# Optimization experiments

Measured on AMD Instinct MI355X. Metric: run time of the kernel, lower is better.

Reference implementation:

```python
import jax, jax.numpy as jnp
import numpy as np

N_USER = 150000
N_RECIPE = 150000
H = 64        # hidden_channels
UF = 58       # user_feat_dim
RF = 128      # recipe_feat_dim
E = 2000000   # rating edges
EL = 500000   # supervision edges


def _lin(k, fan_out, fan_in):
    s = 1.0 / np.sqrt(fan_in)
    kw, kb = jax.random.split(k)
    w = jax.random.uniform(kw, (fan_out, fan_in), jnp.float32, -s, s)
    b = jax.random.uniform(kb, (fan_out,), jnp.float32, -s, s)
    return w, b


def setup_inputs() -> dict:
    key = jax.random.key(0)
    ks = jax.random.split(key, 16)
    inp = {
        'x_user': jax.random.normal(ks[0], (N_USER, UF), jnp.float32),
        'x_recipe': jax.random.normal(ks[1], (N_RECIPE, RF), jnp.float32),
        'user_node_id': jnp.arange(N_USER, dtype=jnp.int64 if jax.config.jax_enable_x64 else jnp.int32),
        'recipe_node_id': jnp.arange(N_RECIPE, dtype=jnp.int64 if jax.config.jax_enable_x64 else jnp.int32),
        'edge_index': jax.random.randint(ks[2], (2, E), 0, N_USER),
        'edge_label_index': jax.random.randint(ks[3], (2, EL), 0, N_USER),
    }
    inp['user_lin_w'], inp['user_lin_b'] = _lin(ks[4], H, UF)
    inp['recipe_lin_w'], inp['recipe_lin_b'] = _lin(ks[5], H, RF)
    inp['user_emb'] = jax.random.normal(ks[6], (N_USER, H), jnp.float32)
    inp['recipe_emb'] = jax.random.normal(ks[7], (N_RECIPE, H), jnp.float32)
    # SAGEConv per layer (1,2) per relation (rates: user->recipe, rev: recipe->user)
    i = 8
    for layer in (1, 2):
        for rel in ('rates', 'rev'):
            wl, bl = _lin(ks[i], H, H)
            wr, _ = _lin(ks[i + 1], H, H)  # lin_r has no bias in PyG SAGEConv
            inp[f'c{layer}_{rel}_wl'] = wl
            inp[f'c{layer}_{rel}_bl'] = bl
            inp[f'c{layer}_{rel}_wr'] = wr
            i += 2
    return inp


def sage_conv(x_src, x_dst, src, dst, wl, bl, wr, n_dst):
    # PyG SAGEConv: lin_l(mean of neighbor messages) + lin_r(self)
    msg = x_src[src]                                              # [E, H] gather
    summed = jax.ops.segment_sum(msg, dst, num_segments=n_dst)    # [n_dst, H]
    cnt = jax.ops.segment_sum(jnp.ones((src.shape[0],), x_src.dtype), dst,
                              num_segments=n_dst)
    mean = summed / jnp.maximum(cnt, 1.0)[:, None]
    return mean @ wl.T + bl + x_dst @ wr.T


def reference(x_user, x_recipe, user_node_id, recipe_node_id, edge_index,
              edge_label_index, user_lin_w, user_lin_b, recipe_lin_w,
              recipe_lin_b, user_emb, recipe_emb,
              c1_rates_wl, c1_rates_bl, c1_rates_wr,
              c1_rev_wl, c1_rev_bl, c1_rev_wr,
              c2_rates_wl, c2_rates_bl, c2_rates_wr,
              c2_rev_wl, c2_rev_bl, c2_rev_wr):
    # Input encoders: linear + embedding lookup
    xu = x_user @ user_lin_w.T + user_lin_b + user_emb[user_node_id]
    xr = x_recipe @ recipe_lin_w.T + recipe_lin_b + recipe_emb[recipe_node_id]

    u_src, r_dst = edge_index[0], edge_index[1]

    # Layer 1 (hetero: each node type receives from exactly one relation)
    hr = sage_conv(xu, xr, u_src, r_dst, c1_rates_wl, c1_rates_bl, c1_rates_wr, N_RECIPE)
    hu = sage_conv(xr, xu, r_dst, u_src, c1_rev_wl, c1_rev_bl, c1_rev_wr, N_USER)
    hu, hr = jax.nn.relu(hu), jax.nn.relu(hr)

    # Layer 2
    hr2 = sage_conv(hu, hr, u_src, r_dst, c2_rates_wl, c2_rates_bl, c2_rates_wr, N_RECIPE)
    hu2 = sage_conv(hr, hu, r_dst, u_src, c2_rev_wl, c2_rev_bl, c2_rev_wr, N_USER)

    # Dot-product edge classifier
    return (hu2[edge_label_index[0]] * hr2[edge_label_index[1]]).sum(axis=-1)
```

## Files before the change

kernel.cpp:

```cpp
#include <hip/hip_runtime.h>
#include <hip/hip_fp16.h>

constexpr int NU = 150000;
constexpr int NR = 150000;
constexpr int Hc = 64;
constexpr int UF = 58;
constexpr int RF = 128;
constexpr long EE = 2000000;
constexpr long ELc = 500000;
constexpr int NTOT = NU + NR;
constexpr int BKT = 256;
constexpr int NB_R = (NR + BKT - 1) / BKT;
constexpr int NB_U = (NU + BKT - 1) / BKT;
constexpr int NBKT = NB_R + NB_U;
constexpr int CHUNK = 4096;
constexpr int NCHUNK = (int)((EE + CHUNK - 1) / CHUNK);
constexpr int NTILE = NU / 16;
constexpr int GB8 = (NU / 8 + 3) / 4;

typedef _Float16 f16;
typedef f16 f16x8 __attribute__((ext_vector_type(8)));
typedef float f32x4 __attribute__((ext_vector_type(4)));

__global__ void bucket_count_kernel(const int* __restrict__ ei, int* __restrict__ bcnt) {
    __shared__ int lc[NBKT];
    for (int i = threadIdx.x; i < NBKT; i += 256) lc[i] = 0;
    __syncthreads();
    long e0 = (long)blockIdx.x * CHUNK;
    for (int k = threadIdx.x; k < CHUNK; k += 256) {
        long e = e0 + k;
        if (e < EE) {
            int u = ei[e], r = ei[EE + e];
            atomicAdd(&lc[r >> 8], 1);
            atomicAdd(&lc[NB_R + (u >> 8)], 1);
        }
    }
    __syncthreads();
    for (int i = threadIdx.x; i < NBKT; i += 256)
        if (lc[i]) atomicAdd(&bcnt[i], lc[i]);
}

__global__ void bucket_scan_kernel(const int* __restrict__ bcnt, int* __restrict__ bbase,
                                   int* __restrict__ bcur) {
    __shared__ int part[256];
    constexpr int PER = (NBKT + 255) / 256;
    int t = threadIdx.x;
    int loc[PER];
    int sum = 0;
    for (int j = 0; j < PER; ++j) {
        int i = t * PER + j;
        int v = (i < NBKT) ? bcnt[i] : 0;
        loc[j] = sum;
        sum += v;
    }
    part[t] = sum;
    __syncthreads();
    for (int off = 1; off < 256; off <<= 1) {
        int v = (t >= off) ? part[t - off] : 0;
        __syncthreads();
        part[t] += v;
        __syncthreads();
    }
    int pre = (t == 0) ? 0 : part[t - 1];
    for (int j = 0; j < PER; ++j) {
        int i = t * PER + j;
        if (i < NBKT) {
            int b = pre + loc[j];
            bbase[i] = b;
            bcur[i] = b;
        }
    }
    if (t == 255) bbase[NBKT] = part[255];
}

__global__ void scatter_records_kernel(const int* __restrict__ ei, int* __restrict__ bcur,
                                       int* __restrict__ rec) {
    __shared__ int lc[NBKT];
    for (int i = threadIdx.x; i < NBKT; i += 256) lc[i] = 0;
    __syncthreads();
    long e0 = (long)blockIdx.x * CHUNK;
    for (int k = threadIdx.x; k < CHUNK; k += 256) {
        long e = e0 + k;
        if (e < EE) {
            int u = ei[e], r = ei[EE + e];
            atomicAdd(&lc[r >> 8], 1);
            atomicAdd(&lc[NB_R + (u >> 8)], 1);
        }
    }
    __syncthreads();
    for (int i = threadIdx.x; i < NBKT; i += 256) {
        int c = lc[i];
        lc[i] = c ? atomicAdd(&bcur[i], c) : 0;
    }
    __syncthreads();
    for (int k = threadIdx.x; k < CHUNK; k += 256) {
        long e = e0 + k;
        if (e < EE) {
            int u = ei[e], r = ei[EE + e];
            int p1 = atomicAdd(&lc[r >> 8], 1);
            rec[p1] = ((r & 255) << 18) | u;
            int p2 = atomicAdd(&lc[NB_R + (u >> 8)], 1);
            rec[p2] = ((u & 255) << 18) | r;
        }
    }
}

__global__ void build_adj_kernel(const int* __restrict__ rec, const int* __restrict__ bbase,
                                 int* __restrict__ adj, int* __restrict__ base,
                                 int* __restrict__ cnt) {
    __shared__ int c256[BKT];
    __shared__ int off256[BKT];
    int b = blockIdx.x;
    int s = bbase[b], e = bbase[b + 1];
    int t = threadIdx.x;
    c256[t] = 0;
    __syncthreads();
    for (int k = s + t; k < e; k += 256) atomicAdd(&c256[rec[k] >> 18], 1);
    __syncthreads();
    int v = c256[t];
    off256[t] = v;
    __syncthreads();
    for (int off = 1; off < 256; off <<= 1) {
        int x = (t >= off) ? off256[t - off] : 0;
        __syncthreads();
        off256[t] += x;
        __syncthreads();
    }
    int excl = off256[t] - v;
    bool isU = (b >= NB_R);
    int node = (isU ? (b - NB_R) : b) * BKT + t;
    int lim = isU ? NU : NR;
    if (node < lim) {
        int cid = isU ? (NR + node) : node;
        base[cid] = s + excl;
        cnt[cid] = v;
    }
    c256[t] = s + excl;
    __syncthreads();
    for (int k = s + t; k < e; k += 256) {
        int rv = rec[k];
        int p = atomicAdd(&c256[rv >> 18], 1);
        adj[p] = rv & 0x3FFFF;
    }
}

template <int F>
__global__ __launch_bounds__(256) void encode_mfma(
        const float* __restrict__ xin, const float* __restrict__ w,
        const float* __restrict__ b, const float* __restrict__ emb,
        const int* __restrict__ nid, __half* __restrict__ out) {
    constexpr int KT = (F + 31) / 32;
    __shared__ f16 wlds[Hc * F];
    for (int i = threadIdx.x; i < Hc * F; i += 256) wlds[i] = (f16)w[i];
    __syncthreads();
    int l = threadIdx.x & 63;
    int m = l & 15;
    int g = l >> 4;
    f16x8 bf[4][KT];
#pragma unroll
    for (int ct = 0; ct < 4; ++ct)
#pragma unroll
        for (int kt = 0; kt < KT; ++kt)
#pragma unroll
            for (int j = 0; j < 8; ++j) {
                int k = kt * 32 + g * 8 + j;
                bf[ct][kt][j] = (k < F) ? wlds[(ct * 16 + m) * F + k] : (f16)0.0f;
            }
    float bv[4];
#pragma unroll
    for (int ct = 0; ct < 4; ++ct) bv[ct] = b[ct * 16 + m];
    int wid0 = (int)(((long)blockIdx.x * 256 + threadIdx.x) >> 6);
    int nw = (gridDim.x * 256) >> 6;
    for (int rt = wid0; rt < NTILE; rt += nw) {
        int r0 = rt * 16;
        const float* xrow = xin + (long)(r0 + m) * F;
        f16x8 af[KT];
#pragma unroll
        for (int kt = 0; kt < KT; ++kt)
#pragma unroll
            for (int jj = 0; jj < 4; ++jj) {
                int k = kt * 32 + g * 8 + jj * 2;
                if (k + 1 < F) {
                    float2 v = *(const float2*)(xrow + k);
                    af[kt][jj * 2] = (f16)v.x;
                    af[kt][jj * 2 + 1] = (f16)v.y;
                } else {
                    af[kt][jj * 2] = (k < F) ? (f16)xrow[k] : (f16)0.0f;
                    af[kt][jj * 2 + 1] = (f16)0.0f;
                }
            }
        f32x4 acc[4] = {{0,0,0,0},{0,0,0,0},{0,0,0,0},{0,0,0,0}};
#pragma unroll
        for (int ct = 0; ct < 4; ++ct)
#pragma unroll
            for (int kt = 0; kt < KT; ++kt)
                acc[ct] = __builtin_amdgcn_mfma_f32_16x16x32_f16(af[kt], bf[ct][kt], acc[ct], 0, 0, 0);
#pragma unroll
        for (int q = 0; q < 4; ++q) {
            int r = r0 + g * 4 + q;
            long ebase = (long)nid[r] * Hc;
#pragma unroll
            for (int ct = 0; ct < 4; ++ct) {
                int col = ct * 16 + m;
                float v = acc[ct][q] + bv[ct] + emb[ebase + col];
                out[(long)r * Hc + col] = __float2half(v);
            }
        }
    }
}

__global__ __launch_bounds__(256) void dense2_mfma(
        const __half* inU, const float* wlU, const float* brU, const float* wrU,
        __half* ToutU, __half* PREU,
        const __half* inR, const float* wlR, const float* brR, const float* wrR,
        __half* ToutR, __half* PRER) {
    __shared__ f16 wlds[2][Hc * Hc];
    int half = gridDim.x >> 1;
    bool isR = blockIdx.x >= half;
    const __half* in = isR ? inR : inU;
    const float* wl = isR ? wlR : wlU;
    const float* wr = isR ? wrR : wrU;
    const float* br = isR ? brR : brU;
    __half* Tout = isR ? ToutR : ToutU;
    __half* PRE  = isR ? PRER : PREU;
    for (int i = threadIdx.x; i < Hc * Hc; i += 256) {
        wlds[0][i] = (f16)wl[i];
        wlds[1][i] = (f16)wr[i];
    }
    __syncthreads();
    int l = threadIdx.x & 63;
    int m = l & 15;
    int g = l >> 4;
    f16x8 bf[8][2];
#pragma unroll
    for (int ct = 0; ct < 4; ++ct)
#pragma unroll
        for (int kt = 0; kt < 2; ++kt) {
            bf[ct][kt]     = *(const f16x8*)&wlds[0][(ct * 16 + m) * Hc + kt * 32 + g * 8];
            bf[4 + ct][kt] = *(const f16x8*)&wlds[1][(ct * 16 + m) * Hc + kt * 32 + g * 8];
        }
    float bv[4];
#pragma unroll
    for (int ct = 0; ct < 4; ++ct) bv[ct] = br[ct * 16 + m];
    int wid0 = (int)((((long)blockIdx.x - (isR ? half : 0)) * 256 + threadIdx.x) >> 6);
    int nw = (half * 256) >> 6;
    for (int rt = wid0; rt < NTILE; rt += nw) {
        int r0 = rt * 16;
        f16x8 af[2];
        const __half* irow = in + (long)(r0 + m) * Hc;
        af[0] = *(const f16x8*)(irow + g * 8);
        af[1] = *(const f16x8*)(irow + 32 + g * 8);
        f32x4 acc[8] = {{0,0,0,0},{0,0,0,0},{0,0,0,0},{0,0,0,0},
                        {0,0,0,0},{0,0,0,0},{0,0,0,0},{0,0,0,0}};
#pragma unroll
        for (int ct = 0; ct < 8; ++ct)
#pragma unroll
            for (int kt = 0; kt < 2; ++kt)
                acc[ct] = __builtin_amdgcn_mfma_f32_16x16x32_f16(af[kt], bf[ct][kt], acc[ct], 0, 0, 0);
#pragma unroll
        for (int q = 0; q < 4; ++q) {
            int r = r0 + g * 4 + q;
#pragma unroll
            for (int ct = 0; ct < 4; ++ct) {
                int col = ct * 16 + m;
                Tout[(long)r * Hc + col] = __float2half(acc[ct][q]);
                PRE[(long)r * Hc + col] = __float2half(acc[4 + ct][q] + bv[ct]);
            }
        }
    }
}

__global__ __launch_bounds__(256) void gather8_kernel(
        const __half* __restrict__ TA, __half* __restrict__ ioA,
        const __half* __restrict__ TB, __half* __restrict__ ioB,
        const int* __restrict__ base, const int* __restrict__ cnt,
        const int* __restrict__ adj, int relu) {
    int l = threadIdx.x & 63;
    int d = l >> 3;
    int o = l & 7;
    int half = gridDim.x >> 1;
    bool isU = blockIdx.x >= half;
    int bid = blockIdx.x - (isU ? half : 0);
    int wid = bid * 4 + (threadIdx.x >> 6);
    int r = wid * 8 + d;
    if (r >= NU) return;
    int noff = isU ? NR : 0;
    const __half* T = isU ? TB : TA;
    __half* io = isU ? ioB : ioA;
    int b0 = base[noff + r], c = cnt[noff + r];
    int co = o * 8;
    __half2 z = __float2half2_rn(0.0f);
    __half2 s0 = z, s1 = z, s2 = z, s3 = z;
    __half2 t0 = z, t1 = z, t2 = z, t3 = z;
    int j = 0;
    for (; j + 1 < c; j += 2) {
        int n0 = adj[b0 + j];
        int n1 = adj[b0 + j + 1];
        uint4 v0 = *(const uint4*)(T + n0 * Hc + co);
        uint4 v1 = *(const uint4*)(T + n1 * Hc + co);
        s0 = __hadd2(s0, *(__half2*)&v0.x); t0 = __hadd2(t0, *(__half2*)&v1.x);
        s1 = __hadd2(s1, *(__half2*)&v0.y); t1 = __hadd2(t1, *(__half2*)&v1.y);
        s2 = __hadd2(s2, *(__half2*)&v0.z); t2 = __hadd2(t2, *(__half2*)&v1.z);
        s3 = __hadd2(s3, *(__half2*)&v0.w); t3 = __hadd2(t3, *(__half2*)&v1.w);
    }
    if (j < c) {
        int n = adj[b0 + j];
        uint4 v = *(const uint4*)(T + n * Hc + co);
        s0 = __hadd2(s0, *(__half2*)&v.x);
        s1 = __hadd2(s1, *(__half2*)&v.y);
        s2 = __hadd2(s2, *(__half2*)&v.z);
        s3 = __hadd2(s3, *(__half2*)&v.w);
    }
    s0 = __hadd2(s0, t0); s1 = __hadd2(s1, t1);
    s2 = __hadd2(s2, t2); s3 = __hadd2(s3, t3);
    float inv = 1.0f / fmaxf((float)c, 1.0f);
    __half* op = io + (long)r * Hc + co;
    uint4 cur = *(const uint4*)op;
    __half2 acc[4] = {s0, s1, s2, s3};
    unsigned int* cw = &cur.x;
    uint4 outv;
    unsigned int* ow = &outv.x;
#pragma unroll
    for (int q = 0; q < 4; ++q) {
        float2 f = __half22float2(*(__half2*)&cw[q]);
        float2 a = __half22float2(acc[q]);
        float ox = f.x + a.x * inv;
        float oy = f.y + a.y * inv;
        if (relu) { ox = fmaxf(ox, 0.0f); oy = fmaxf(oy, 0.0f); }
        __half2 h = __floats2half2_rn(ox, oy);
        ow[q] = *(unsigned int*)&h;
    }
    *(uint4*)op = outv;
}

__global__ void edge_dot_kernel(const int* __restrict__ eli,
                                const __half* __restrict__ HU2, const __half* __restrict__ HR2,
                                float* __restrict__ out) {
    long gid = (long)blockIdx.x * blockDim.x + threadIdx.x;
    long e = gid >> 4;
    int t = (int)(gid & 15);
    if (e >= ELc) return;
    int a = eli[e], b = eli[ELc + e];
    const __half2* xa = (const __half2*)(HU2 + (long)a * Hc + t * 4);
    const __half2* yb = (const __half2*)(HR2 + (long)b * Hc + t * 4);
    float2 x0 = __half22float2(xa[0]), x1 = __half22float2(xa[1]);
    float2 y0 = __half22float2(yb[0]), y1 = __half22float2(yb[1]);
    float v = x0.x * y0.x + x0.y * y0.y + x1.x * y1.x + x1.y * y1.y;
    v += __shfl_xor(v, 1);
    v += __shfl_xor(v, 2);
    v += __shfl_xor(v, 4);
    v += __shfl_xor(v, 8);
    if (t == 0) out[e] = v;
}

extern "C" void kernel_launch(void* const* d_in, const int* in_sizes, int n_in,
                              void* d_out, int out_size, void* d_ws, size_t ws_size,
                              hipStream_t stream) {
    const float* x_user   = (const float*)d_in[0];
    const float* x_recipe = (const float*)d_in[1];
    const int*   user_nid = (const int*)d_in[2];
    const int*   rec_nid  = (const int*)d_in[3];
    const int*   edge_index = (const int*)d_in[4];
    const int*   edge_label = (const int*)d_in[5];
    const float* u_w   = (const float*)d_in[6];
    const float* u_b   = (const float*)d_in[7];
    const float* r_w   = (const float*)d_in[8];
    const float* r_b   = (const float*)d_in[9];
    const float* u_emb = (const float*)d_in[10];
    const float* r_emb = (const float*)d_in[11];
    const float* c1ra_wl = (const float*)d_in[12];
    const float* c1ra_bl = (const float*)d_in[13];
    const float* c1ra_wr = (const float*)d_in[14];
    const float* c1rv_wl = (const float*)d_in[15];
    const float* c1rv_bl = (const float*)d_in[16];
    const float* c1rv_wr = (const float*)d_in[17];
    const float* c2ra_wl = (const float*)d_in[18];
    const float* c2ra_bl = (const float*)d_in[19];
    const float* c2ra_wr = (const float*)d_in[20];
    const float* c2rv_wl = (const float*)d_in[21];
    const float* c2rv_bl = (const float*)d_in[22];
    const float* c2rv_wr = (const float*)d_in[23];

    const long NH = (long)NU * Hc;
    __half* B0 = (__half*)d_ws;
    __half* B1 = B0 + NH;
    __half* B2 = B1 + NH;
    __half* B3 = B2 + NH;
    __half* TAh = B3 + NH;
    __half* TBh = TAh + NH;
    int* cnt   = (int*)(TBh + NH);
    int* base  = cnt + NTOT;
    int* bcnt  = base + NTOT;
    int* bbase = bcnt + NBKT;
    int* bcur  = bbase + NBKT + 1;
    int* adj   = bcur + NBKT;
    int* rec = (int*)B2;

    hipMemsetAsync(bcnt, 0, (size_t)NBKT * sizeof(int), stream);
    bucket_count_kernel<<<NCHUNK, 256, 0, stream>>>(edge_index, bcnt);
    bucket_scan_kernel<<<1, 256, 0, stream>>>(bcnt, bbase, bcur);
    scatter_records_kernel<<<NCHUNK, 256, 0, stream>>>(edge_index, bcur, rec);
    build_adj_kernel<<<NBKT, 256, 0, stream>>>(rec, bbase, adj, base, cnt);

    encode_mfma<UF><<<1024, 256, 0, stream>>>(x_user, u_w, u_b, u_emb, user_nid, B0);
    encode_mfma<RF><<<1024, 256, 0, stream>>>(x_recipe, r_w, r_b, r_emb, rec_nid, B1);

    dense2_mfma<<<2048, 256, 0, stream>>>(
        B0, c1ra_wl, c1rv_bl, c1rv_wr, TAh, B2,
        B1, c1rv_wl, c1ra_bl, c1ra_wr, TBh, B3);

    gather8_kernel<<<2 * GB8, 256, 0, stream>>>(TAh, B3, TBh, B2, base, cnt, adj, 1);

    dense2_mfma<<<2048, 256, 0, stream>>>(
        B2, c2ra_wl, c2rv_bl, c2rv_wr, TAh, B0,
        B3, c2rv_wl, c2ra_bl, c2ra_wr, TBh, B1);

    gather8_kernel<<<2 * GB8, 256, 0, stream>>>(TAh, B1, TBh, B0, base, cnt, adj, 0);

    edge_dot_kernel<<<(ELc * 16) / 256, 256, 0, stream>>>(edge_label, B0, B1, (float*)d_out);
}
```

Before: 409.9 us.

## Sort adjacency lists and unroll gather accumulation by four

Adds a per-node insertion sort of each adjacency list so neighbour gathers walk memory in ascending index order, aiming for better cache locality. The gather loop is unrolled to four independent accumulators for more memory-level parallelism, and the destination row load is hoisted before the loop so its latency overlaps with the gathers. The sort is an extra kernel that runs one thread per node over roughly 13-entry lists in global memory, so its added time may offset the gains. Summation order in fp16 also changes slightly.

```diff
diff --git a/kernel.cpp b/kernel.cpp
--- a/kernel.cpp
+++ b/kernel.cpp
@@ -141,6 +141,22 @@
         int rv = rec[k];
         int p = atomicAdd(&c256[rv >> 18], 1);
         adj[p] = rv & 0x3FFFF;
+    }
+}
+
+__global__ void sort_adj_kernel(int* __restrict__ adj, const int* __restrict__ base,
+                                const int* __restrict__ cnt) {
+    int i = blockIdx.x * blockDim.x + threadIdx.x;
+    if (i >= NTOT) return;
+    int s = base[i], c = cnt[i];
+    for (int a = 1; a < c; ++a) {
+        int key = adj[s + a];
+        int j = a - 1;
+        while (j >= 0 && adj[s + j] > key) {
+            adj[s + j + 1] = adj[s + j];
+            --j;
+        }
+        adj[s + j + 1] = key;
     }
 }
 
@@ -289,21 +305,33 @@
     __half* io = isU ? ioB : ioA;
     int b0 = base[noff + r], c = cnt[noff + r];
     int co = o * 8;
+    __half* op = io + (long)r * Hc + co;
+    uint4 cur = *(const uint4*)op;
     __half2 z = __float2half2_rn(0.0f);
     __half2 s0 = z, s1 = z, s2 = z, s3 = z;
     __half2 t0 = z, t1 = z, t2 = z, t3 = z;
+    __half2 u0 = z, u1 = z, u2 = z, u3 = z;
+    __half2 w0 = z, w1 = z, w2 = z, w3 = z;
     int j = 0;
-    for (; j + 1 < c; j += 2) {
+    for (; j + 3 < c; j += 4) {
         int n0 = adj[b0 + j];
         int n1 = adj[b0 + j + 1];
+        int n2 = adj[b0 + j + 2];
+        int n3 = adj[b0 + j + 3];
         uint4 v0 = *(const uint4*)(T + n0 * Hc + co);
         uint4 v1 = *(const uint4*)(T + n1 * Hc + co);
+        uint4 v2 = *(const uint4*)(T + n2 * Hc + co);
+        uint4 v3 = *(const uint4*)(T + n3 * Hc + co);
         s0 = __hadd2(s0, *(__half2*)&v0.x); t0 = __hadd2(t0, *(__half2*)&v1.x);
+        u0 = __hadd2(u0, *(__half2*)&v2.x); w0 = __hadd2(w0, *(__half2*)&v3.x);
         s1 = __hadd2(s1, *(__half2*)&v0.y); t1 = __hadd2(t1, *(__half2*)&v1.y);
+        u1 = __hadd2(u1, *(__half2*)&v2.y); w1 = __hadd2(w1, *(__half2*)&v3.y);
         s2 = __hadd2(s2, *(__half2*)&v0.z); t2 = __hadd2(t2, *(__half2*)&v1.z);
+        u2 = __hadd2(u2, *(__half2*)&v2.z); w2 = __hadd2(w2, *(__half2*)&v3.z);
         s3 = __hadd2(s3, *(__half2*)&v0.w); t3 = __hadd2(t3, *(__half2*)&v1.w);
-    }
-    if (j < c) {
+        u3 = __hadd2(u3, *(__half2*)&v2.w); w3 = __hadd2(w3, *(__half2*)&v3.w);
+    }
+    for (; j < c; ++j) {
         int n = adj[b0 + j];
         uint4 v = *(const uint4*)(T + n * Hc + co);
         s0 = __hadd2(s0, *(__half2*)&v.x);
@@ -311,11 +339,11 @@
         s2 = __hadd2(s2, *(__half2*)&v.z);
         s3 = __hadd2(s3, *(__half2*)&v.w);
     }
-    s0 = __hadd2(s0, t0); s1 = __hadd2(s1, t1);
-    s2 = __hadd2(s2, t2); s3 = __hadd2(s3, t3);
+    s0 = __hadd2(__hadd2(s0, t0), __hadd2(u0, w0));
+    s1 = __hadd2(__hadd2(s1, t1), __hadd2(u1, w1));
+    s2 = __hadd2(__hadd2(s2, t2), __hadd2(u2, w2));
+    s3 = __hadd2(__hadd2(s3, t3), __hadd2(u3, w3));
     float inv = 1.0f / fmaxf((float)c, 1.0f);
-    __half* op = io + (long)r * Hc + co;
-    uint4 cur = *(const uint4*)op;
     __half2 acc[4] = {s0, s1, s2, s3};
     unsigned int* cw = &cur.x;
     uint4 outv;
@@ -401,6 +429,7 @@
     bucket_scan_kernel<<<1, 256, 0, stream>>>(bcnt, bbase, bcur);
     scatter_records_kernel<<<NCHUNK, 256, 0, stream>>>(edge_index, bcur, rec);
     build_adj_kernel<<<NBKT, 256, 0, stream>>>(rec, bbase, adj, base, cnt);
+    sort_adj_kernel<<<(NTOT + 255) / 256, 256, 0, stream>>>(adj, base, cnt);
 
     encode_mfma<UF><<<1024, 256, 0, stream>>>(x_user, u_w, u_b, u_emb, user_nid, B0);
     encode_mfma<RF><<<1024, 256, 0, stream>>>(x_recipe, r_w, r_b, r_emb, rec_nid, B1);
```

Result: slower. 541.4 us (+32.1%).
